# Performance work log

Measured on AMD Instinct MI355X. Metric: run time of the kernel, lower is better.

## Reference

```python
import jax, jax.numpy as jnp
import numpy as np

N_NODES = 100000
N_EDGES = 1600000
IN_DIM = 128
HIDDEN = 128
OUT_DIM = 10
N_GRAPHS = 512
N_LAYERS = 3


def setup_inputs() -> dict:
    key = jax.random.key(0)
    ks = jax.random.split(key, 12)
    s_in = 1.0 / np.sqrt(IN_DIM)
    s_h = 1.0 / np.sqrt(HIDDEN)
    return {
        "x": jax.random.normal(ks[0], (N_NODES, IN_DIM), jnp.float32),
        "lin1_w": jax.random.normal(ks[1], (IN_DIM, HIDDEN), jnp.float32) * s_in,
        "lin1_b": jnp.zeros((HIDDEN,), jnp.float32),
        "gcn_w": jax.random.normal(ks[2], (N_LAYERS, HIDDEN, HIDDEN), jnp.float32) * s_h,
        "gcn_b": jnp.zeros((N_LAYERS, HIDDEN), jnp.float32),
        "lin_out_w": jax.random.normal(ks[3], (HIDDEN, HIDDEN), jnp.float32) * s_h,
        "lin_out_b": jnp.zeros((HIDDEN,), jnp.float32),
        "cls_w": jax.random.normal(ks[4], (HIDDEN, OUT_DIM), jnp.float32) * s_h,
        "cls_b": jnp.zeros((OUT_DIM,), jnp.float32),
        "edge_index": jax.random.randint(ks[5], (2, N_EDGES), 0, N_NODES, jnp.int64),
        "batch": jnp.sort(jax.random.randint(ks[6], (N_NODES,), 0, N_GRAPHS, jnp.int64)),
    }


def reference(x, lin1_w, lin1_b, gcn_w, gcn_b, lin_out_w, lin_out_b, cls_w, cls_b, edge_index, batch):
    n = x.shape[0]
    # GCNConv normalization with added self-loops (PyG default)
    row, col = edge_index[0], edge_index[1]
    loop = jnp.arange(n)
    row2 = jnp.concatenate([row, loop])  # source (message origin)
    col2 = jnp.concatenate([col, loop])  # target (aggregation index)
    deg = jax.ops.segment_sum(jnp.ones_like(col2, dtype=x.dtype), col2, num_segments=n)
    dinv = jax.lax.rsqrt(jnp.maximum(deg, 1.0))
    norm = (dinv[row2] * dinv[col2])[:, None]  # [E+N, 1]

    counts = jax.ops.segment_sum(jnp.ones((n,), x.dtype), batch, num_segments=N_GRAPHS)
    counts = jnp.maximum(counts, 1.0)[:, None]

    def readout_mean(h):  # global_mean_pool -> [G, H]
        return jax.ops.segment_sum(h, batch, num_segments=N_GRAPHS) / counts

    # lin1 + elu (dropout = identity in eval mode)
    h = jax.nn.elu(x @ lin1_w + lin1_b)
    reps = readout_mean(h)  # readout_layers[0]; l_sum accumulates layer reps
    for i in range(N_LAYERS):
        hw = h @ gcn_w[i]                       # [N, H]
        msg = norm * hw[row2]                   # gather + scale
        agg = jax.ops.segment_sum(msg, col2, num_segments=n)  # scatter-add
        h = jax.nn.elu(agg + gcn_b[i])          # GCNConv bias then NaOp act
        # pooling op is 'none' (remove_pooling=True): graph unchanged
        reps = reps + readout_mean(h)           # readout_layers[i+1], summed by LaOp 'l_sum'
    g = jax.nn.elu(reps @ lin_out_w + lin_out_b)
    logits = g @ cls_w + cls_b
    return jax.nn.log_softmax(logits, axis=-1)
```

## Files before the change

### kernel.cpp

```cpp
#include <hip/hip_runtime.h>
#include <hip/hip_bf16.h>
#include <math.h>

#define NN 100000
#define NE 1600000
#define HID 128
#define NG 512
#define NB 512
#define RB 196

typedef unsigned short ushort_t;
typedef __attribute__((ext_vector_type(8))) short bf16x8;
typedef __attribute__((ext_vector_type(8))) unsigned short ushort8_t;
typedef __attribute__((ext_vector_type(4))) float f32x4;

__device__ __forceinline__ ushort_t f2bf(float v) {
    unsigned u = __float_as_uint(v);
    unsigned r = (u + 0x7FFF + ((u >> 16) & 1)) >> 16;
    return (ushort_t)r;
}
__device__ __forceinline__ float bf2f(ushort_t u) {
    return __uint_as_float((unsigned)u << 16);
}

__global__ __launch_bounds__(256) void hist_and_prepw(const int* __restrict__ ecol, int* __restrict__ ghist, int E,
                                                      const float* __restrict__ lin1_w,
                                                      const float* __restrict__ gcn_w,
                                                      ushort_t* __restrict__ wt_hi,
                                                      ushort_t* __restrict__ wt_lo) {
    if (blockIdx.x < 512) {
        __shared__ int lh[NB];
        for (int i = threadIdx.x; i < NB; i += 256) lh[i] = 0;
        __syncthreads();
        for (int e = blockIdx.x * 256 + threadIdx.x; e < E; e += 512 * 256)
            atomicAdd(&lh[ecol[e] / RB], 1);
        __syncthreads();
        for (int i = threadIdx.x; i < NB; i += 256) {
            int c = lh[i];
            if (c) atomicAdd(&ghist[i], c);
        }
    } else {
        int mb = blockIdx.x - 512;
        int m = mb >> 3;
        int chunk = mb & 7;
        const float* W = (m == 0) ? lin1_w : gcn_w + (size_t)(m - 1) * 16384;
        ushort_t* hi = wt_hi + (size_t)m * 16384;
        ushort_t* lo = wt_lo + (size_t)m * 16384;
        for (int i = chunk * 2048 + threadIdx.x; i < (chunk + 1) * 2048; i += 256) {
            int j = i & 7;
            int lane = (i >> 3) & 63;
            int ks = (i >> 9) & 3;
            int ct = (i >> 11) & 7;
            int n = ct * 16 + (lane & 15);
            int k = ks * 32 + (lane >> 4) * 8 + j;
            float v = W[k * 128 + n];
            ushort_t h = f2bf(v);
            hi[i] = h;
            lo[i] = f2bf(v - bf2f(h));
        }
    }
}

__global__ __launch_bounds__(NB) void bucket_scan(const int* __restrict__ ghist, int* __restrict__ brp,
                                                  int* __restrict__ gcur, int* __restrict__ rp) {
    __shared__ int s[NB];
    int t = threadIdx.x;
    int v = ghist[t];
    s[t] = v;
    __syncthreads();
    for (int off = 1; off < NB; off <<= 1) {
        int x = (t >= off) ? s[t - off] : 0;
        __syncthreads();
        s[t] += x;
        __syncthreads();
    }
    int ex = s[t] - v;
    brp[t] = ex;
    gcur[t] = ex;
    if (t == NB - 1) { brp[NB] = s[t]; rp[NN] = s[t]; }
}

#define CHUNK 4096
__global__ __launch_bounds__(256) void partition_edges(const int* __restrict__ erow, const int* __restrict__ ecol,
                                                       int* __restrict__ gcur, unsigned int* __restrict__ pairs, int E) {
    __shared__ int cnt[NB];
    __shared__ int base[NB];
    const int t = threadIdx.x;
    const int e0 = blockIdx.x * CHUNK;
    const int e1 = min(e0 + CHUNK, E);
    for (int i = t; i < NB; i += 256) cnt[i] = 0;
    __syncthreads();
    for (int e = e0 + t; e < e1; e += 256) atomicAdd(&cnt[ecol[e] / RB], 1);
    __syncthreads();
    for (int i = t; i < NB; i += 256) {
        int c = cnt[i];
        base[i] = c ? atomicAdd(&gcur[i], c) : 0;
        cnt[i] = 0;
    }
    __syncthreads();
    for (int e = e0 + t; e < e1; e += 256) {
        int d = ecol[e];
        int b = d / RB;
        int off = atomicAdd(&cnt[b], 1);
        pairs[base[b] + off] = ((unsigned)erow[e] << 8) | (unsigned)(d - b * RB);
    }
}

__global__ __launch_bounds__(256) void bucket_fill(const unsigned int* __restrict__ pairs, const int* __restrict__ brp,
                                                   int* __restrict__ rp, float* __restrict__ dinv,
                                                   int* __restrict__ csrc) {
    __shared__ int cnt[RB];
    __shared__ int cur[RB];
    __shared__ int sc[256];
    const int b = blockIdx.x, t = threadIdx.x;
    const int nbase = b * RB;
    const int s = brp[b], e = brp[b + 1];
    for (int i = t; i < RB; i += 256) cnt[i] = 0;
    __syncthreads();
    for (int i = s + t; i < e; i += 256) atomicAdd(&cnt[pairs[i] & 255u], 1);
    __syncthreads();
    int v = (t < RB) ? cnt[t] : 0;
    sc[t] = v;
    __syncthreads();
    for (int off = 1; off < 256; off <<= 1) {
        int x = (t >= off) ? sc[t - off] : 0;
        __syncthreads();
        sc[t] += x;
        __syncthreads();
    }
    if (t < RB) {
        int ex = s + sc[t] - v;
        int node = nbase + t;
        if (node < NN) {
            rp[node] = ex;
            dinv[node] = rsqrtf((float)v + 1.0f);
        }
        cur[t] = ex;
    }
    __syncthreads();
    for (int i = s + t; i < e; i += 256) {
        unsigned int p = pairs[i];
        int slot = atomicAdd(&cur[p & 255u], 1);
        csrc[slot] = (int)(p >> 8);
    }
}

template<bool F32A, int MODE>
__global__ __launch_bounds__(256) void gemm_mfma(const float* __restrict__ A,
                                                 const ushort_t* __restrict__ a_bf,
                                                 const ushort_t* __restrict__ wt_hi,
                                                 const ushort_t* __restrict__ wt_lo,
                                                 const float* __restrict__ bias,
                                                 const float* __restrict__ dinv,
                                                 ushort_t* __restrict__ out0,
                                                 int N) {
    const int lane = threadIdx.x & 63;
    const int wid = threadIdx.x >> 6;
    const int rowBase = blockIdx.x * 128 + wid * 32;
    const int l15 = lane & 15, lg = lane >> 4;

    f32x4 acc[2][8];
#pragma unroll
    for (int rt = 0; rt < 2; ++rt)
#pragma unroll
        for (int ct = 0; ct < 8; ++ct) acc[rt][ct] = (f32x4){0.f, 0.f, 0.f, 0.f};

#pragma unroll
    for (int ks = 0; ks < 4; ++ks) {
        bf16x8 ahi[2], alo[2];
#pragma unroll
        for (int rt = 0; rt < 2; ++rt) {
            int r = rowBase + rt * 16 + l15;
            if (F32A) {
                float av[8];
                if (r < N) {
                    const float* ap = A + (size_t)r * 128 + ks * 32 + lg * 8;
                    float4 a0 = *(const float4*)(ap);
                    float4 a1 = *(const float4*)(ap + 4);
                    av[0] = a0.x; av[1] = a0.y; av[2] = a0.z; av[3] = a0.w;
                    av[4] = a1.x; av[5] = a1.y; av[6] = a1.z; av[7] = a1.w;
                } else {
#pragma unroll
                    for (int j = 0; j < 8; ++j) av[j] = 0.f;
                }
#pragma unroll
                for (int j = 0; j < 8; ++j) {
                    ushort_t h = f2bf(av[j]);
                    ahi[rt][j] = (short)h;
                    alo[rt][j] = (short)f2bf(av[j] - bf2f(h));
                }
            } else {
                if (r < N) {
                    ahi[rt] = *(const bf16x8*)(a_bf + (size_t)r * 128 + ks * 32 + lg * 8);
                } else {
                    bf16x8 z = {0, 0, 0, 0, 0, 0, 0, 0};
                    ahi[rt] = z;
                }
            }
        }
#pragma unroll
        for (int ct = 0; ct < 8; ++ct) {
            size_t boff = (size_t)(((ct * 4 + ks) * 64 + lane) * 8);
            bf16x8 bhi = *(const bf16x8*)(wt_hi + boff);
            bf16x8 blo = *(const bf16x8*)(wt_lo + boff);
            acc[0][ct] = __builtin_amdgcn_mfma_f32_16x16x32_bf16(ahi[0], bhi, acc[0][ct], 0, 0, 0);
            acc[1][ct] = __builtin_amdgcn_mfma_f32_16x16x32_bf16(ahi[1], bhi, acc[1][ct], 0, 0, 0);
            acc[0][ct] = __builtin_amdgcn_mfma_f32_16x16x32_bf16(ahi[0], blo, acc[0][ct], 0, 0, 0);
            acc[1][ct] = __builtin_amdgcn_mfma_f32_16x16x32_bf16(ahi[1], blo, acc[1][ct], 0, 0, 0);
            if (F32A) {
                acc[0][ct] = __builtin_amdgcn_mfma_f32_16x16x32_bf16(alo[0], bhi, acc[0][ct], 0, 0, 0);
                acc[1][ct] = __builtin_amdgcn_mfma_f32_16x16x32_bf16(alo[1], bhi, acc[1][ct], 0, 0, 0);
            }
        }
    }

#pragma unroll
    for (int rt = 0; rt < 2; ++rt) {
#pragma unroll
        for (int reg = 0; reg < 4; ++reg) {
            int row = rowBase + rt * 16 + lg * 4 + reg;
            if (row >= N) continue;
            if (MODE == 0) {
#pragma unroll
                for (int ct = 0; ct < 8; ++ct) {
                    int colc = ct * 16 + l15;
                    float v = acc[rt][ct][reg] + bias[colc];
                    v = v > 0.f ? v : expf(v) - 1.f;
                    out0[(size_t)row * 128 + colc] = f2bf(v);
                }
            } else {
                float dv = dinv[row];
#pragma unroll
                for (int ct = 0; ct < 8; ++ct) {
                    int colc = ct * 16 + l15;
                    out0[(size_t)row * 128 + colc] = f2bf(acc[rt][ct][reg] * dv);
                }
            }
        }
    }
}

__global__ __launch_bounds__(256) void gather_agg(const int* __restrict__ rp,
                                                  const int* __restrict__ csrc,
                                                  const float* __restrict__ dinv,
                                                  const ushort_t* __restrict__ hwb,
                                                  const float* __restrict__ bias,
                                                  ushort_t* __restrict__ h_out) {
    int v = blockIdx.x * 16 + (threadIdx.x >> 4);
    if (v >= NN) return;
    int c8 = (threadIdx.x & 15) << 3;
    int s = rp[v], e = rp[v + 1];
    float acc[8] = {};

    int i = s;
    for (; i + 16 <= e; i += 16) {
        int u[16];
#pragma unroll
        for (int k = 0; k < 16; ++k) u[k] = csrc[i + k];
        ushort8_t r[16];
#pragma unroll
        for (int k = 0; k < 16; ++k) r[k] = *(const ushort8_t*)(hwb + (size_t)u[k] * 128 + c8);
#pragma unroll
        for (int k = 0; k < 16; ++k)
#pragma unroll
            for (int j = 0; j < 8; ++j) acc[j] += bf2f(r[k][j]);
    }
    for (; i + 8 <= e; i += 8) {
        int u[8];
#pragma unroll
        for (int k = 0; k < 8; ++k) u[k] = csrc[i + k];
        ushort8_t r[8];
#pragma unroll
        for (int k = 0; k < 8; ++k) r[k] = *(const ushort8_t*)(hwb + (size_t)u[k] * 128 + c8);
#pragma unroll
        for (int k = 0; k < 8; ++k)
#pragma unroll
            for (int j = 0; j < 8; ++j) acc[j] += bf2f(r[k][j]);
    }
    for (; i < e; ++i) {
        int u = csrc[i];
        ushort8_t r0 = *(const ushort8_t*)(hwb + (size_t)u * 128 + c8);
#pragma unroll
        for (int j = 0; j < 8; ++j) acc[j] += bf2f(r0[j]);
    }

    float di = dinv[v];
    ushort8_t sv = *(const ushort8_t*)(hwb + (size_t)v * 128 + c8);
    ushort8_t o;
#pragma unroll
    for (int j = 0; j < 8; ++j) {
        float t = di * (acc[j] + bf2f(sv[j])) + bias[c8 + j];
        t = t > 0.f ? t : expf(t) - 1.f;
        o[j] = f2bf(t);
    }
    *(ushort8_t*)(h_out + (size_t)v * 128 + c8) = o;
}

__global__ __launch_bounds__(256) void readout(const ushort_t* __restrict__ h,
                                               const int* __restrict__ batch,
                                               int n, float* __restrict__ reps) {
    int g = blockIdx.x >> 2;
    int part = blockIdx.x & 3;
    int lo = 0, hi = n;
    while (lo < hi) { int m = (lo + hi) >> 1; if (batch[m] < g) lo = m + 1; else hi = m; }
    int s = lo;
    lo = 0; hi = n;
    while (lo < hi) { int m = (lo + hi) >> 1; if (batch[m] < g + 1) lo = m + 1; else hi = m; }
    int e = lo;

    __shared__ float sh[16][128];
    int ns = threadIdx.x >> 4;
    int L  = threadIdx.x & 15;
    int c8 = L << 3;
    float acc[8] = {};
    for (int v = s + part + ns * 4; v < e; v += 64) {
        ushort8_t t = *(const ushort8_t*)(h + (size_t)v * 128 + c8);
#pragma unroll
        for (int j = 0; j < 8; ++j) acc[j] += bf2f(t[j]);
    }
#pragma unroll
    for (int j = 0; j < 8; ++j) sh[ns][c8 + j] = acc[j];
    __syncthreads();
    if (threadIdx.x < 128) {
        int c = threadIdx.x;
        float sum = 0.f;
#pragma unroll
        for (int k = 0; k < 16; ++k) sum += sh[k][c];
        float cnt = (float)(e - s > 0 ? e - s : 1);
        unsafeAtomicAdd(&reps[(size_t)g * 128 + c], sum / cnt);
    }
}

__global__ __launch_bounds__(256) void gemm128(const float* __restrict__ A,
                                               const float* __restrict__ W,
                                               const float* __restrict__ bias,
                                               float* __restrict__ out,
                                               int N, int applyElu) {
    __shared__ float xs[64][128];
    __shared__ float ws[128][64];
    const int tid = threadIdx.x;
    const int rowBase = blockIdx.x * 64;
    const int colBase = blockIdx.y * 64;
#pragma unroll
    for (int it = 0; it < 8; ++it) {
        int idx = it * 256 + tid;
        int r = idx >> 5;
        int c4 = (idx & 31) << 2;
        int gr = rowBase + r;
        float4 v = make_float4(0.f, 0.f, 0.f, 0.f);
        if (gr < N) v = *(const float4*)(A + (size_t)gr * 128 + c4);
        *(float4*)(&xs[r][c4]) = v;
    }
#pragma unroll
    for (int it = 0; it < 8; ++it) {
        int idx = it * 256 + tid;
        int k = idx >> 4;
        int c4 = (idx & 15) << 2;
        *(float4*)(&ws[k][c4]) = *(const float4*)(W + (size_t)k * 128 + colBase + c4);
    }
    __syncthreads();
    const int rowg = tid >> 4, colg = tid & 15;
    const int r0 = rowg * 4, c0 = colg * 4;
    float acc[4][4] = {};
#pragma unroll 2
    for (int kb = 0; kb < 128; kb += 4) {
        float4 xr[4], wr[4];
#pragma unroll
        for (int i = 0; i < 4; ++i) xr[i] = *(const float4*)(&xs[r0 + i][kb]);
#pragma unroll
        for (int kk = 0; kk < 4; ++kk) wr[kk] = *(const float4*)(&ws[kb + kk][c0]);
#pragma unroll
        for (int i = 0; i < 4; ++i) {
            const float* xp = (const float*)&xr[i];
#pragma unroll
            for (int kk = 0; kk < 4; ++kk) {
                float xv = xp[kk];
                acc[i][0] = fmaf(xv, wr[kk].x, acc[i][0]);
                acc[i][1] = fmaf(xv, wr[kk].y, acc[i][1]);
                acc[i][2] = fmaf(xv, wr[kk].z, acc[i][2]);
                acc[i][3] = fmaf(xv, wr[kk].w, acc[i][3]);
            }
        }
    }
    float4 b4 = make_float4(0.f, 0.f, 0.f, 0.f);
    if (bias) b4 = *(const float4*)(bias + colBase + c0);
#pragma unroll
    for (int i = 0; i < 4; ++i) {
        int gr = rowBase + r0 + i;
        if (gr < N) {
            float4 o;
            o.x = acc[i][0] + b4.x;
            o.y = acc[i][1] + b4.y;
            o.z = acc[i][2] + b4.z;
            o.w = acc[i][3] + b4.w;
            if (applyElu) {
                o.x = o.x > 0.f ? o.x : expf(o.x) - 1.f;
                o.y = o.y > 0.f ? o.y : expf(o.y) - 1.f;
                o.z = o.z > 0.f ? o.z : expf(o.z) - 1.f;
                o.w = o.w > 0.f ? o.w : expf(o.w) - 1.f;
            }
            *(float4*)(out + (size_t)gr * 128 + colBase + c0) = o;
        }
    }
}

__global__ __launch_bounds__(64) void cls_logsoftmax(const float* __restrict__ g,
                                                     const float* __restrict__ cw,
                                                     const float* __restrict__ cb,
                                                     float* __restrict__ out) {
    int r = blockIdx.x;
    __shared__ float row[128];
    __shared__ float lg[10];
    int t = threadIdx.x;
    row[t] = g[(size_t)r * 128 + t];
    row[64 + t] = g[(size_t)r * 128 + 64 + t];
    __syncthreads();
    if (t < 10) {
        float a = cb[t];
        for (int k = 0; k < 128; ++k) a = fmaf(row[k], cw[k * 10 + t], a);
        lg[t] = a;
    }
    __syncthreads();
    if (t == 0) {
        float m = lg[0];
#pragma unroll
        for (int j = 1; j < 10; ++j) m = fmaxf(m, lg[j]);
        float se = 0.f;
#pragma unroll
        for (int j = 0; j < 10; ++j) se += expf(lg[j] - m);
        float L = logf(se);
#pragma unroll
        for (int j = 0; j < 10; ++j) out[(size_t)r * 10 + j] = lg[j] - m - L;
    }
}

extern "C" void kernel_launch(void* const* d_in, const int* in_sizes, int n_in,
                              void* d_out, int out_size, void* d_ws, size_t ws_size,
                              hipStream_t stream) {
    const float* x        = (const float*)d_in[0];
    const float* lin1_w   = (const float*)d_in[1];
    const float* lin1_b   = (const float*)d_in[2];
    const float* gcn_w    = (const float*)d_in[3];
    const float* gcn_b    = (const float*)d_in[4];
    const float* lin_out_w= (const float*)d_in[5];
    const float* lin_out_b= (const float*)d_in[6];
    const float* cls_w    = (const float*)d_in[7];
    const float* cls_b    = (const float*)d_in[8];
    const int*   ei       = (const int*)d_in[9];
    const int*   batch    = (const int*)d_in[10];
    float* out = (float*)d_out;

    const int* erow = ei;
    const int* ecol = ei + NE;

    ushort_t* h     = (ushort_t*)d_ws;
    ushort_t* hwb   = h + (size_t)NN * 128;
    float*    dinv  = (float*)(hwb + (size_t)NN * 128);
    float*    reps  = dinv + NN;
    float*    gbuf  = reps + (size_t)NG * 128;
    int*      rp    = (int*)(gbuf + (size_t)NG * 128);
    int*      csrc  = rp + NN + 1;
    int*      ghist = csrc + NE;
    int*      brp   = ghist + NB;
    int*      gcur  = brp + NB + 1;
    ushort_t* wt_hi = (ushort_t*)(gcur + NB);
    ushort_t* wt_lo = wt_hi + 4 * 16384;
    unsigned int* pairs = (unsigned int*)(wt_lo + 4 * 16384);

    hipMemsetAsync(ghist, 0, NB * sizeof(int), stream);
    hipMemsetAsync(reps, 0, (size_t)NG * 128 * sizeof(float), stream);

    hist_and_prepw<<<512 + 32, 256, 0, stream>>>(ecol, ghist, NE, lin1_w, gcn_w, wt_hi, wt_lo);
    bucket_scan<<<1, NB, 0, stream>>>(ghist, brp, gcur, rp);
    partition_edges<<<(NE + CHUNK - 1) / CHUNK, 256, 0, stream>>>(erow, ecol, gcur, pairs, NE);
    bucket_fill<<<NB, 256, 0, stream>>>(pairs, brp, rp, dinv, csrc);

    const int GEMM_GRID = (NN + 127) / 128;

    gemm_mfma<true, 0><<<GEMM_GRID, 256, 0, stream>>>(x, nullptr, wt_hi, wt_lo,
                                                      lin1_b, dinv, h, NN);
    readout<<<NG * 4, 256, 0, stream>>>(h, batch, NN, reps);

    for (int i = 0; i < 3; ++i) {
        gemm_mfma<false, 1><<<GEMM_GRID, 256, 0, stream>>>(nullptr, h,
                                                           wt_hi + (size_t)(i + 1) * 16384,
                                                           wt_lo + (size_t)(i + 1) * 16384,
                                                           nullptr, dinv, hwb, NN);
        gather_agg<<<(NN + 15) / 16, 256, 0, stream>>>(rp, csrc, dinv, hwb,
                                                       gcn_b + (size_t)i * 128, h);
        readout<<<NG * 4, 256, 0, stream>>>(h, batch, NN, reps);
    }

    dim3 gs((NG + 63) / 64, 2);
    gemm128<<<gs, 256, 0, stream>>>(reps, lin_out_w, lin_out_b, gbuf, NG, 1);
    cls_logsoftmax<<<NG, 64, 0, stream>>>(gbuf, cls_w, cls_b, out);
}
```

Baseline: 455.4 us.

## Fuse mean-pool readout into gather_agg epilogue with per-graph segmented atomics

Removes the separate readout kernel after each GCN layer. gather_agg now reduces its 16 nodes' fp32 outputs in shared memory, runs a segmented sum over the sorted batch ids, and atomically adds the scaled sums into reps. Per-graph inverse counts are precomputed in bucket_scan. This avoids re-reading h three times and saves three launches, at the cost of one block-wide sync, extra atomics (about 6250 blocks × 128) and a shared-memory epilogue in the gather kernel.

```diff
diff --git a/kernel.cpp b/kernel.cpp
--- a/kernel.cpp
+++ b/kernel.cpp
@@ -62,7 +62,8 @@
 }
 
 __global__ __launch_bounds__(NB) void bucket_scan(const int* __restrict__ ghist, int* __restrict__ brp,
-                                                  int* __restrict__ gcur, int* __restrict__ rp) {
+                                                  int* __restrict__ gcur, int* __restrict__ rp,
+                                                  const int* __restrict__ batch, float* __restrict__ invcnt) {
     __shared__ int s[NB];
     int t = threadIdx.x;
     int v = ghist[t];
@@ -78,6 +79,14 @@
     brp[t] = ex;
     gcur[t] = ex;
     if (t == NB - 1) { brp[NB] = s[t]; rp[NN] = s[t]; }
+
+    int lo = 0, hi = NN;
+    while (lo < hi) { int m = (lo + hi) >> 1; if (batch[m] < t) lo = m + 1; else hi = m; }
+    int s0 = lo;
+    lo = 0; hi = NN;
+    while (lo < hi) { int m = (lo + hi) >> 1; if (batch[m] < t + 1) lo = m + 1; else hi = m; }
+    int c = lo - s0;
+    invcnt[t] = 1.0f / (float)(c > 0 ? c : 1);
 }
 
 #define CHUNK 4096
@@ -245,55 +254,93 @@
                                                   const float* __restrict__ dinv,
                                                   const ushort_t* __restrict__ hwb,
                                                   const float* __restrict__ bias,
+                                                  const int* __restrict__ batch,
+                                                  const float* __restrict__ invcnt,
+                                                  float* __restrict__ reps,
                                                   ushort_t* __restrict__ h_out) {
-    int v = blockIdx.x * 16 + (threadIdx.x >> 4);
-    if (v >= NN) return;
-    int c8 = (threadIdx.x & 15) << 3;
-    int s = rp[v], e = rp[v + 1];
+    __shared__ float sh[16][128];
+    __shared__ int gid[16];
+    const int v0 = blockIdx.x * 16;
+    const int ns = (int)(threadIdx.x >> 4);
+    int v = v0 + ns;
+    int c8 = (int)(threadIdx.x & 15) << 3;
+    if (threadIdx.x < 16) {
+        int bidx = v0 + (int)threadIdx.x;
+        if (bidx > NN - 1) bidx = NN - 1;
+        gid[threadIdx.x] = batch[bidx];
+    }
+
     float acc[8] = {};
-
-    int i = s;
-    for (; i + 16 <= e; i += 16) {
-        int u[16];
-#pragma unroll
-        for (int k = 0; k < 16; ++k) u[k] = csrc[i + k];
-        ushort8_t r[16];
-#pragma unroll
-        for (int k = 0; k < 16; ++k) r[k] = *(const ushort8_t*)(hwb + (size_t)u[k] * 128 + c8);
-#pragma unroll
-        for (int k = 0; k < 16; ++k)
-#pragma unroll
-            for (int j = 0; j < 8; ++j) acc[j] += bf2f(r[k][j]);
-    }
-    for (; i + 8 <= e; i += 8) {
-        int u[8];
-#pragma unroll
-        for (int k = 0; k < 8; ++k) u[k] = csrc[i + k];
-        ushort8_t r[8];
-#pragma unroll
-        for (int k = 0; k < 8; ++k) r[k] = *(const ushort8_t*)(hwb + (size_t)u[k] * 128 + c8);
-#pragma unroll
-        for (int k = 0; k < 8; ++k)
-#pragma unroll
-            for (int j = 0; j < 8; ++j) acc[j] += bf2f(r[k][j]);
-    }
-    for (; i < e; ++i) {
-        int u = csrc[i];
-        ushort8_t r0 = *(const ushort8_t*)(hwb + (size_t)u * 128 + c8);
-#pragma unroll
-        for (int j = 0; j < 8; ++j) acc[j] += bf2f(r0[j]);
-    }
-
-    float di = dinv[v];
-    ushort8_t sv = *(const ushort8_t*)(hwb + (size_t)v * 128 + c8);
-    ushort8_t o;
-#pragma unroll
-    for (int j = 0; j < 8; ++j) {
-        float t = di * (acc[j] + bf2f(sv[j])) + bias[c8 + j];
-        t = t > 0.f ? t : expf(t) - 1.f;
-        o[j] = f2bf(t);
-    }
-    *(ushort8_t*)(h_out + (size_t)v * 128 + c8) = o;
+    if (v < NN) {
+        int s = rp[v], e = rp[v + 1];
+        int i = s;
+        for (; i + 16 <= e; i += 16) {
+            int u[16];
+#pragma unroll
+            for (int k = 0; k < 16; ++k) u[k] = csrc[i + k];
+            ushort8_t r[16];
+#pragma unroll
+            for (int k = 0; k < 16; ++k) r[k] = *(const ushort8_t*)(hwb + (size_t)u[k] * 128 + c8);
+#pragma unroll
+            for (int k = 0; k < 16; ++k)
+#pragma unroll
+                for (int j = 0; j < 8; ++j) acc[j] += bf2f(r[k][j]);
+        }
+        for (; i + 8 <= e; i += 8) {
+            int u[8];
+#pragma unroll
+            for (int k = 0; k < 8; ++k) u[k] = csrc[i + k];
+            ushort8_t r[8];
+#pragma unroll
+            for (int k = 0; k < 8; ++k) r[k] = *(const ushort8_t*)(hwb + (size_t)u[k] * 128 + c8);
+#pragma unroll
+            for (int k = 0; k < 8; ++k)
+#pragma unroll
+                for (int j = 0; j < 8; ++j) acc[j] += bf2f(r[k][j]);
+        }
+        for (; i < e; ++i) {
+            int u = csrc[i];
+            ushort8_t r0 = *(const ushort8_t*)(hwb + (size_t)u * 128 + c8);
+#pragma unroll
+            for (int j = 0; j < 8; ++j) acc[j] += bf2f(r0[j]);
+        }
+
+        float di = dinv[v];
+        ushort8_t sv = *(const ushort8_t*)(hwb + (size_t)v * 128 + c8);
+        ushort8_t o;
+#pragma unroll
+        for (int j = 0; j < 8; ++j) {
+            float t = di * (acc[j] + bf2f(sv[j])) + bias[c8 + j];
+            t = t > 0.f ? t : expf(t) - 1.f;
+            acc[j] = t;
+            o[j] = f2bf(t);
+        }
+        *(ushort8_t*)(h_out + (size_t)v * 128 + c8) = o;
+    } else {
+#pragma unroll
+        for (int j = 0; j < 8; ++j) acc[j] = 0.f;
+    }
+
+#pragma unroll
+    for (int j = 0; j < 8; ++j) sh[ns][c8 + j] = acc[j];
+    __syncthreads();
+    if (threadIdx.x < 128) {
+        int c = (int)threadIdx.x;
+        int nvalid = NN - v0;
+        if (nvalid > 16) nvalid = 16;
+        float run = sh[0][c];
+        int cg = gid[0];
+        for (int k = 1; k < nvalid; ++k) {
+            int g2 = gid[k];
+            if (g2 != cg) {
+                unsafeAtomicAdd(&reps[(size_t)cg * 128 + c], run * invcnt[cg]);
+                run = 0.f;
+                cg = g2;
+            }
+            run += sh[k][c];
+        }
+        unsafeAtomicAdd(&reps[(size_t)cg * 128 + c], run * invcnt[cg]);
+    }
 }
 
 __global__ __launch_bounds__(256) void readout(const ushort_t* __restrict__ h,
@@ -309,8 +356,8 @@
     int e = lo;
 
     __shared__ float sh[16][128];
-    int ns = threadIdx.x >> 4;
-    int L  = threadIdx.x & 15;
+    int ns = (int)(threadIdx.x >> 4);
+    int L  = (int)(threadIdx.x & 15);
     int c8 = L << 3;
     float acc[8] = {};
     for (int v = s + part + ns * 4; v < e; v += 64) {
@@ -322,7 +369,7 @@
     for (int j = 0; j < 8; ++j) sh[ns][c8 + j] = acc[j];
     __syncthreads();
     if (threadIdx.x < 128) {
-        int c = threadIdx.x;
+        int c = (int)threadIdx.x;
         float sum = 0.f;
 #pragma unroll
         for (int k = 0; k < 16; ++k) sum += sh[k][c];
@@ -458,7 +505,8 @@
     float*    dinv  = (float*)(hwb + (size_t)NN * 128);
     float*    reps  = dinv + NN;
     float*    gbuf  = reps + (size_t)NG * 128;
-    int*      rp    = (int*)(gbuf + (size_t)NG * 128);
+    float*    invcnt= gbuf + (size_t)NG * 128;
+    int*      rp    = (int*)(invcnt + NG);
     int*      csrc  = rp + NN + 1;
     int*      ghist = csrc + NE;
     int*      brp   = ghist + NB;
@@ -471,7 +519,7 @@
     hipMemsetAsync(reps, 0, (size_t)NG * 128 * sizeof(float), stream);
 
     hist_and_prepw<<<512 + 32, 256, 0, stream>>>(ecol, ghist, NE, lin1_w, gcn_w, wt_hi, wt_lo);
-    bucket_scan<<<1, NB, 0, stream>>>(ghist, brp, gcur, rp);
+    bucket_scan<<<1, NB, 0, stream>>>(ghist, brp, gcur, rp, batch, invcnt);
     partition_edges<<<(NE + CHUNK - 1) / CHUNK, 256, 0, stream>>>(erow, ecol, gcur, pairs, NE);
     bucket_fill<<<NB, 256, 0, stream>>>(pairs, brp, rp, dinv, csrc);
 
@@ -487,8 +535,8 @@
                                                            wt_lo + (size_t)(i + 1) * 16384,
                                                            nullptr, dinv, hwb, NN);
         gather_agg<<<(NN + 15) / 16, 256, 0, stream>>>(rp, csrc, dinv, hwb,
-                                                       gcn_b + (size_t)i * 128, h);
-        readout<<<NG * 4, 256, 0, stream>>>(h, batch, NN, reps);
+                                                       gcn_b + (size_t)i * 128,
+                                                       batch, invcnt, reps, h);
     }
 
     dim3 gs((NG + 63) / 64, 2);
```

New measurement: 449.9 us. Within noise of the previous version (-1.2%).
